# Performance work log

Measured on AMD Instinct MI355X. Metric: run time of the kernel, lower is better.

Reference implementation:

```python
import jax, jax.numpy as jnp
import numpy as np

WIN = (16, 9, 9)
WIN_SIZE = WIN[0] * WIN[1] * WIN[2]  # 1296
EPS = float(np.e ** -15)             # ~3.06e-7, matches np.power(np.e, -15)


def setup_inputs() -> dict:
    key = jax.random.key(0)
    k1, k2 = jax.random.split(key)
    shape = (2, 1, 96, 192, 192)  # [B, 1, D, H, W]
    I = jax.random.normal(k1, shape, dtype=jnp.float32)
    J = jax.random.normal(k2, shape, dtype=jnp.float32)
    return {"I": I, "J": J}


def _box_sums(tmp):
    # Grouped conv3d with an all-ones [5,1,16,9,9] kernel: per-channel sliding
    k = jnp.ones((5, 1) + WIN, dtype=tmp.dtype)
    return jax.lax.conv_general_dilated(
        tmp, k,
        window_strides=(1, 1, 1),
        padding=[(0, 0), (WIN[1] // 2, WIN[1] // 2), (WIN[2] // 2, WIN[2] // 2)],
        feature_group_count=5,
        dimension_numbers=("NCDHW", "OIDHW", "NCDHW"),
    )


def reference(I, J):
    # I, J: [B, 1, D, H, W]
    tmp = jnp.concatenate([I, J, I * I, J * J, I * J], axis=1)  # [B,5,D,H,W]
    sums = _box_sums(tmp)  # [B, 5, D-15, H, W]
    I_sum, J_sum = sums[:, 0], sums[:, 1]
    I2_sum, J2_sum, IJ_sum = sums[:, 2], sums[:, 3], sums[:, 4]

    u_I = I_sum / WIN_SIZE
    u_J = J_sum / WIN_SIZE

    cross = IJ_sum - u_J * I_sum - u_I * J_sum + u_I * u_J * WIN_SIZE
    I_var = I2_sum - 2.0 * u_I * I_sum + u_I * u_I * WIN_SIZE
    J_var = J2_sum - 2.0 * u_J * J_sum + u_J * u_J * WIN_SIZE

    nz = (I_var * J_var) > EPS  # bool_non_zero; where false, substitute 1.0
    cross = jnp.where(nz, cross, 1.0)
    I_var = jnp.where(nz, I_var, 1.0)
    J_var = jnp.where(nz, J_var, 1.0)

    cc = cross * cross / (I_var * J_var + EPS)  # [B, D-15, H, W]
    loss = -1.0 * jnp.mean(cc, axis=(1, 2, 3)) + 1.0  # [B]
    return loss, cc
```

## Files before the change

### kernel.cpp

```cpp
#include <hip/hip_runtime.h>


constexpr int N = 2, D = 96, H = 192, W = 192;
constexpr int OD = 81;
constexpr int KD = 16;
constexpr int HWp = H * W;
constexpr float INV_WIN = 1.0f / 1296.0f;
constexpr float EPS_NZ = 3.0590232050182579e-07f;
constexpr int CH = 24;
constexpr int ODPB = 27;

__device__ __forceinline__ unsigned bf16rne(float f) {
  unsigned u = __float_as_uint(f);
  return (u + 0x7fffu + ((u >> 16) & 1u)) >> 16;
}
__device__ __forceinline__ float bf16tof(unsigned h) {
  return __uint_as_float(h << 16);
}

__global__ __launch_bounds__(192)
void k_dw(const float* __restrict__ I, const float* __restrict__ J,
          unsigned* __restrict__ ws, int od0, int c, int odcStride) {
  const int h = blockIdx.x;
  const int n = blockIdx.z;
  const int os = od0 + blockIdx.y * ODPB;
  int oe = od0 + c; if (os + ODPB < oe) oe = os + ODPB;
  if (os >= oe) return;
  const int w = threadIdx.x;

  __shared__ float4 x4[W + 8];
  __shared__ float  x1[W + 8];
  __shared__ float4 a4[W + 8];
  __shared__ float  a1[W + 8];

  if (w < 4)       { x4[w]     = make_float4(0.f,0.f,0.f,0.f); x1[w]     = 0.f; }
  if (w >= W - 4)  { x4[w + 8] = make_float4(0.f,0.f,0.f,0.f); x1[w + 8] = 0.f; }
  __syncthreads();

  const size_t colBase = ((size_t)n * D * H + h) * (size_t)W + w;
  const float* Ip = I + colBase;
  const float* Jp = J + colBase;
  unsigned* wbase = ws + ((size_t)n * odcStride * HWp + (size_t)h * W + w) * 3;

  int pe = -1;
  if (w < 3) pe = w + 1;
  else if (w >= W - 3) pe = w + 7;

  const int dEnd = oe + KD - 1;
  float sI = 0.f, sJ = 0.f, sII = 0.f, sJJ = 0.f, sIJ = 0.f;
  float ivN = Ip[(size_t)os * HWp];
  float jvN = Jp[(size_t)os * HWp];
  float ioN = 0.f, joN = 0.f;

  for (int d = os; d < dEnd; ++d) {
    const float iv = ivN, jv = jvN;
    const float io = ioN, jo = joN;
    const int dn = d + 1;
    if (dn < dEnd) {
      ivN = Ip[(size_t)dn * HWp];
      jvN = Jp[(size_t)dn * HWp];
      if (dn >= os + KD - 1) {
        const int odn = dn - (KD - 1);
        ioN = Ip[(size_t)odn * HWp];
        joN = Jp[(size_t)odn * HWp];
      }
    }
    sI += iv; sJ += jv;
    sII += iv * iv; sJJ += jv * jv; sIJ += iv * jv;
    if (d >= os + KD - 1) {
      const int od = d - (KD - 1);
      const int p = 4 + w;
      __builtin_amdgcn_s_barrier();
      x4[p] = make_float4(sI, sJ, sII, sJJ); x1[p] = sIJ;
      asm volatile("s_waitcnt lgkmcnt(0)" ::: "memory");
      __builtin_amdgcn_s_barrier();
      {
        float4 m0 = x4[p - 1], m1 = x4[p], m2 = x4[p + 1];
        a4[p] = make_float4(m0.x + m1.x + m2.x, m0.y + m1.y + m2.y,
                            m0.z + m1.z + m2.z, m0.w + m1.w + m2.w);
        a1[p] = x1[p - 1] + x1[p] + x1[p + 1];
        if (pe >= 0) {
          float4 e0 = x4[pe - 1], e1 = x4[pe], e2 = x4[pe + 1];
          a4[pe] = make_float4(e0.x + e1.x + e2.x, e0.y + e1.y + e2.y,
                               e0.z + e1.z + e2.z, e0.w + e1.w + e2.w);
          a1[pe] = x1[pe - 1] + x1[pe] + x1[pe + 1];
        }
      }
      asm volatile("s_waitcnt lgkmcnt(0)" ::: "memory");
      __builtin_amdgcn_s_barrier();
      float4 b0 = a4[p - 3], b1 = a4[p], b2 = a4[p + 3];
      const float r0 = b0.x + b1.x + b2.x;
      const float r1 = b0.y + b1.y + b2.y;
      const float r2 = b0.z + b1.z + b2.z;
      const float r3 = b0.w + b1.w + b2.w;
      const float r4 = a1[p - 3] + a1[p] + a1[p + 3];
      unsigned* o = wbase + (size_t)(od - od0) * HWp * 3;
      uint3 v = make_uint3(bf16rne(r0) | (bf16rne(r1) << 16),
                           bf16rne(r2) | (bf16rne(r3) << 16),
                           bf16rne(r4));
      *(uint3*)o = v;
      sI -= io; sJ -= jo;
      sII -= io * io; sJJ -= jo * jo; sIJ -= io * jo;
    }
  }
}

__global__ __launch_bounds__(192)
void k_hcc(const unsigned* __restrict__ ws, float* __restrict__ cc,
           float* __restrict__ acc, int od0, int odcStride) {
  const int odi = blockIdx.x;
  const int od = od0 + odi;
  const int h0 = blockIdx.y * CH;
  const int n = blockIdx.z;
  const int w = threadIdx.x;
  const unsigned* base =
      ws + ((size_t)n * odcStride * HWp + (size_t)odi * HWp + w) * 3;
  float* ccp = cc + ((size_t)n * OD + od) * (size_t)HWp + w;

  float s0 = 0.f, s1 = 0.f, s2 = 0.f, s3 = 0.f, s4 = 0.f;
  float lsum = 0.f;
  uint3 hist[8];
  const uint3 z3 = make_uint3(0u, 0u, 0u);

  uint3 vN = z3;
  {
    const int hin = h0 - 4;
    if (hin >= 0) vN = *(const uint3*)(base + (size_t)hin * W * 3);
  }
#pragma unroll
  for (int t = 0; t < CH + 8; ++t) {
    const uint3 v = vN;
    if (t + 1 < CH + 8) {
      const int hn = h0 - 4 + t + 1;
      vN = (hn >= 0 && hn < H) ? *(const uint3*)(base + (size_t)hn * W * 3) : z3;
    }
    s0 += bf16tof(v.x & 0xffffu); s1 += bf16tof(v.x >> 16);
    s2 += bf16tof(v.y & 0xffffu); s3 += bf16tof(v.y >> 16);
    s4 += bf16tof(v.z & 0xffffu);
    if (t >= 8) {
      const int h = h0 + t - 8;
      const float cross = s4 - s0 * s1 * INV_WIN;
      const float vI = s2 - s0 * s0 * INV_WIN;
      const float vJ = s3 - s1 * s1 * INV_WIN;
      const float prod = vI * vJ;
      const float c = (prod > EPS_NZ) ? (cross * cross) / (prod + EPS_NZ)
                                      : 1.0f / (1.0f + EPS_NZ);
      ccp[(size_t)h * W] = c;
      lsum += c;
      const uint3 q = hist[t & 7];
      s0 -= bf16tof(q.x & 0xffffu); s1 -= bf16tof(q.x >> 16);
      s2 -= bf16tof(q.y & 0xffffu); s3 -= bf16tof(q.y >> 16);
      s4 -= bf16tof(q.z & 0xffffu);
    }
    hist[t & 7] = v;
  }
  __shared__ float red[3];
#pragma unroll
  for (int off = 32; off > 0; off >>= 1) lsum += __shfl_xor(lsum, off, 64);
  if ((threadIdx.x & 63) == 0) red[threadIdx.x >> 6] = lsum;
  __syncthreads();
  if (threadIdx.x == 0) atomicAdd(acc + n, red[0] + red[1] + red[2]);
}

__global__ void k_fin(const float* __restrict__ acc, float* __restrict__ out) {
  if (threadIdx.x < N)
    out[threadIdx.x] = 1.0f - acc[threadIdx.x] * (1.0f / 2985984.0f);
}

extern "C" void kernel_launch(void* const* d_in, const int* in_sizes, int n_in,
                              void* d_out, int out_size, void* d_ws,
                              size_t ws_size, hipStream_t stream) {
  const float* I = (const float*)d_in[0];
  const float* J = (const float*)d_in[1];
  float* out = (float*)d_out;
  float* acc = (float*)d_ws;
  unsigned* planes = (unsigned*)((char*)d_ws + 256);

  hipMemsetAsync(d_ws, 0, 2 * sizeof(float), stream);

  const size_t perOdPerN = (size_t)HWp * 12;
  size_t avail = (ws_size > 256) ? (ws_size - 256) : 0;
  long long odcMax = (long long)(avail / (2 * perOdPerN));
  if (odcMax < 1) odcMax = 1;
  if (odcMax > OD) odcMax = OD;
  const int odc = (int)odcMax;

  float* ccOut = out + 2;
  for (int od0 = 0; od0 < OD; od0 += odc) {
    const int c = (odc < OD - od0) ? odc : (OD - od0);
    const int S = (c + ODPB - 1) / ODPB;
    hipLaunchKernelGGL(k_dw, dim3(H, S, N), dim3(192), 0, stream,
                       I, J, planes, od0, c, odc);
    hipLaunchKernelGGL(k_hcc, dim3(c, H / CH, N), dim3(192), 0, stream,
                       planes, ccOut, acc, od0, odc);
  }
  hipLaunchKernelGGL(k_fin, dim3(1), dim3(64), 0, stream, acc, out);
}
```

Measured before the change: 78.79 us.

## Use fp16 packed sums and wave bpermute for W-direction box filter

```diff
diff --git a/kernel.cpp b/kernel.cpp
--- a/kernel.cpp
+++ b/kernel.cpp
@@ -8,17 +8,25 @@
 constexpr float INV_WIN = 1.0f / 1296.0f;
 constexpr float EPS_NZ = 3.0590232050182579e-07f;
 constexpr int CH = 24;
-constexpr int ODPB = 27;
+constexpr int ODPB = 14;
 
-__device__ __forceinline__ unsigned bf16rne(float f) {
-  unsigned u = __float_as_uint(f);
-  return (u + 0x7fffu + ((u >> 16) & 1u)) >> 16;
+typedef __fp16 h2 __attribute__((ext_vector_type(2)));
+
+__device__ __forceinline__ unsigned pkrtz(float lo, float hi) {
+  h2 h = __builtin_amdgcn_cvt_pkrtz(lo, hi);
+  unsigned u; __builtin_memcpy(&u, &h, 4); return u;
 }
-__device__ __forceinline__ float bf16tof(unsigned h) {
-  return __uint_as_float(h << 16);
+__device__ __forceinline__ h2 as_h2(unsigned u) {
+  h2 h; __builtin_memcpy(&h, &u, 4); return h;
+}
+__device__ __forceinline__ unsigned as_u(h2 h) {
+  unsigned u; __builtin_memcpy(&u, &h, 4); return u;
+}
+__device__ __forceinline__ unsigned bperm(int bidx, unsigned v) {
+  return (unsigned)__builtin_amdgcn_ds_bpermute(bidx, (int)v);
 }
 
-__global__ __launch_bounds__(192)
+__global__ __launch_bounds__(256)
 void k_dw(const float* __restrict__ I, const float* __restrict__ J,
           unsigned* __restrict__ ws, int od0, int c, int odcStride) {
   const int h = blockIdx.x;
@@ -26,81 +34,63 @@
   const int os = od0 + blockIdx.y * ODPB;
   int oe = od0 + c; if (os + ODPB < oe) oe = os + ODPB;
   if (os >= oe) return;
-  const int w = threadIdx.x;
 
-  __shared__ float4 x4[W + 8];
-  __shared__ float  x1[W + 8];
-  __shared__ float4 a4[W + 8];
-  __shared__ float  a1[W + 8];
+  const int lane = threadIdx.x & 63;
+  const int seg  = threadIdx.x >> 6;
+  const int wcol = seg * 56 + lane - 4;
+  const bool colOK = (wcol >= 0) && (wcol < W);
+  const bool stOK  = (lane >= 4) && (lane < 60) && (wcol < W);
 
-  if (w < 4)       { x4[w]     = make_float4(0.f,0.f,0.f,0.f); x1[w]     = 0.f; }
-  if (w >= W - 4)  { x4[w + 8] = make_float4(0.f,0.f,0.f,0.f); x1[w + 8] = 0.f; }
-  __syncthreads();
-
-  const size_t colBase = ((size_t)n * D * H + h) * (size_t)W + w;
+  const size_t colBase = ((size_t)n * D * H + h) * (size_t)W + wcol;
   const float* Ip = I + colBase;
   const float* Jp = J + colBase;
-  unsigned* wbase = ws + ((size_t)n * odcStride * HWp + (size_t)h * W + w) * 3;
+  unsigned* wbase = ws + ((size_t)n * odcStride * HWp + (size_t)h * W + wcol) * 3;
 
-  int pe = -1;
-  if (w < 3) pe = w + 1;
-  else if (w >= W - 3) pe = w + 7;
+  const int im1 = ((lane - 1) & 63) << 2;
+  const int ip1 = ((lane + 1) & 63) << 2;
+  const int im3 = ((lane - 3) & 63) << 2;
+  const int ip3 = ((lane + 3) & 63) << 2;
 
-  const int dEnd = oe + KD - 1;
   float sI = 0.f, sJ = 0.f, sII = 0.f, sJJ = 0.f, sIJ = 0.f;
-  float ivN = Ip[(size_t)os * HWp];
-  float jvN = Jp[(size_t)os * HWp];
-  float ioN = 0.f, joN = 0.f;
-
-  for (int d = os; d < dEnd; ++d) {
-    const float iv = ivN, jv = jvN;
-    const float io = ioN, jo = joN;
-    const int dn = d + 1;
-    if (dn < dEnd) {
-      ivN = Ip[(size_t)dn * HWp];
-      jvN = Jp[(size_t)dn * HWp];
-      if (dn >= os + KD - 1) {
-        const int odn = dn - (KD - 1);
-        ioN = Ip[(size_t)odn * HWp];
-        joN = Jp[(size_t)odn * HWp];
-      }
-    }
+  for (int d = os; d < os + KD - 1; ++d) {
+    const float iv = colOK ? Ip[(size_t)d * HWp] : 0.f;
+    const float jv = colOK ? Jp[(size_t)d * HWp] : 0.f;
     sI += iv; sJ += jv;
     sII += iv * iv; sJJ += jv * jv; sIJ += iv * jv;
-    if (d >= os + KD - 1) {
-      const int od = d - (KD - 1);
-      const int p = 4 + w;
-      __builtin_amdgcn_s_barrier();
-      x4[p] = make_float4(sI, sJ, sII, sJJ); x1[p] = sIJ;
-      asm volatile("s_waitcnt lgkmcnt(0)" ::: "memory");
-      __builtin_amdgcn_s_barrier();
-      {
-        float4 m0 = x4[p - 1], m1 = x4[p], m2 = x4[p + 1];
-        a4[p] = make_float4(m0.x + m1.x + m2.x, m0.y + m1.y + m2.y,
-                            m0.z + m1.z + m2.z, m0.w + m1.w + m2.w);
-        a1[p] = x1[p - 1] + x1[p] + x1[p + 1];
-        if (pe >= 0) {
-          float4 e0 = x4[pe - 1], e1 = x4[pe], e2 = x4[pe + 1];
-          a4[pe] = make_float4(e0.x + e1.x + e2.x, e0.y + e1.y + e2.y,
-                               e0.z + e1.z + e2.z, e0.w + e1.w + e2.w);
-          a1[pe] = x1[pe - 1] + x1[pe] + x1[pe + 1];
-        }
-      }
-      asm volatile("s_waitcnt lgkmcnt(0)" ::: "memory");
-      __builtin_amdgcn_s_barrier();
-      float4 b0 = a4[p - 3], b1 = a4[p], b2 = a4[p + 3];
-      const float r0 = b0.x + b1.x + b2.x;
-      const float r1 = b0.y + b1.y + b2.y;
-      const float r2 = b0.z + b1.z + b2.z;
-      const float r3 = b0.w + b1.w + b2.w;
-      const float r4 = a1[p - 3] + a1[p] + a1[p + 3];
+  }
+
+  float eI = colOK ? Ip[(size_t)(os + KD - 1) * HWp] : 0.f;
+  float eJ = colOK ? Jp[(size_t)(os + KD - 1) * HWp] : 0.f;
+  float lI = colOK ? Ip[(size_t)os * HWp] : 0.f;
+  float lJ = colOK ? Jp[(size_t)os * HWp] : 0.f;
+
+  for (int od = os; od < oe; ++od) {
+    const float ceI = eI, ceJ = eJ, clI = lI, clJ = lJ;
+    const int odn = od + 1;
+    if (odn < oe) {
+      eI = colOK ? Ip[(size_t)(odn + KD - 1) * HWp] : 0.f;
+      eJ = colOK ? Jp[(size_t)(odn + KD - 1) * HWp] : 0.f;
+      lI = colOK ? Ip[(size_t)odn * HWp] : 0.f;
+      lJ = colOK ? Jp[(size_t)odn * HWp] : 0.f;
+    }
+    sI += ceI; sJ += ceJ;
+    sII += ceI * ceI; sJJ += ceJ * ceJ; sIJ += ceI * ceJ;
+    const unsigned x0 = pkrtz(sI, sJ);
+    const unsigned x1 = pkrtz(sII, sJJ);
+    const unsigned x2 = pkrtz(sIJ, 0.f);
+    sI -= clI; sJ -= clJ;
+    sII -= clI * clI; sJJ -= clJ * clJ; sIJ -= clI * clJ;
+
+    const unsigned a0 = as_u(as_h2(bperm(im1, x0)) + as_h2(x0) + as_h2(bperm(ip1, x0)));
+    const unsigned a1 = as_u(as_h2(bperm(im1, x1)) + as_h2(x1) + as_h2(bperm(ip1, x1)));
+    const unsigned a2 = as_u(as_h2(bperm(im1, x2)) + as_h2(x2) + as_h2(bperm(ip1, x2)));
+    const unsigned r0 = as_u(as_h2(bperm(im3, a0)) + as_h2(a0) + as_h2(bperm(ip3, a0)));
+    const unsigned r1 = as_u(as_h2(bperm(im3, a1)) + as_h2(a1) + as_h2(bperm(ip3, a1)));
+    const unsigned r2 = as_u(as_h2(bperm(im3, a2)) + as_h2(a2) + as_h2(bperm(ip3, a2)));
+
+    if (stOK) {
       unsigned* o = wbase + (size_t)(od - od0) * HWp * 3;
-      uint3 v = make_uint3(bf16rne(r0) | (bf16rne(r1) << 16),
-                           bf16rne(r2) | (bf16rne(r3) << 16),
-                           bf16rne(r4));
-      *(uint3*)o = v;
-      sI -= io; sJ -= jo;
-      sII -= io * io; sJJ -= jo * jo; sIJ -= io * jo;
+      o[0] = r0; o[1] = r1; o[2] = r2;
     }
   }
 }
@@ -134,9 +124,12 @@
       const int hn = h0 - 4 + t + 1;
       vN = (hn >= 0 && hn < H) ? *(const uint3*)(base + (size_t)hn * W * 3) : z3;
     }
-    s0 += bf16tof(v.x & 0xffffu); s1 += bf16tof(v.x >> 16);
-    s2 += bf16tof(v.y & 0xffffu); s3 += bf16tof(v.y >> 16);
-    s4 += bf16tof(v.z & 0xffffu);
+    {
+      h2 v0 = as_h2(v.x), v1 = as_h2(v.y), v2 = as_h2(v.z);
+      s0 += (float)v0[0]; s1 += (float)v0[1];
+      s2 += (float)v1[0]; s3 += (float)v1[1];
+      s4 += (float)v2[0];
+    }
     if (t >= 8) {
       const int h = h0 + t - 8;
       const float cross = s4 - s0 * s1 * INV_WIN;
@@ -148,9 +141,10 @@
       ccp[(size_t)h * W] = c;
       lsum += c;
       const uint3 q = hist[t & 7];
-      s0 -= bf16tof(q.x & 0xffffu); s1 -= bf16tof(q.x >> 16);
-      s2 -= bf16tof(q.y & 0xffffu); s3 -= bf16tof(q.y >> 16);
-      s4 -= bf16tof(q.z & 0xffffu);
+      h2 q0 = as_h2(q.x), q1 = as_h2(q.y), q2 = as_h2(q.z);
+      s0 -= (float)q0[0]; s1 -= (float)q0[1];
+      s2 -= (float)q1[0]; s3 -= (float)q1[1];
+      s4 -= (float)q2[0];
     }
     hist[t & 7] = v;
   }
@@ -189,7 +183,7 @@
   for (int od0 = 0; od0 < OD; od0 += odc) {
     const int c = (odc < OD - od0) ? odc : (OD - od0);
     const int S = (c + ODPB - 1) / ODPB;
-    hipLaunchKernelGGL(k_dw, dim3(H, S, N), dim3(192), 0, stream,
+    hipLaunchKernelGGL(k_dw, dim3(H, S, N), dim3(256), 0, stream,
                        I, J, planes, od0, c, odc);
     hipLaunchKernelGGL(k_hcc, dim3(c, H / CH, N), dim3(192), 0, stream,
                        planes, ccOut, acc, od0, odc);
```

Result: faster. 76.73 us (-2.6%).

## Move W-direction box sum from depth kernel into H/cc kernel, split atomics

Applied to the files above, without the earlier changes.

```diff
diff --git a/kernel.cpp b/kernel.cpp
--- a/kernel.cpp
+++ b/kernel.cpp
@@ -8,7 +8,7 @@
 constexpr float INV_WIN = 1.0f / 1296.0f;
 constexpr float EPS_NZ = 3.0590232050182579e-07f;
 constexpr int CH = 24;
-constexpr int ODPB = 27;
+constexpr int ODPB = 14;
 
 __device__ __forceinline__ unsigned bf16rne(float f) {
   unsigned u = __float_as_uint(f);
@@ -19,8 +19,8 @@
 }
 
 __global__ __launch_bounds__(192)
-void k_dw(const float* __restrict__ I, const float* __restrict__ J,
-          unsigned* __restrict__ ws, int od0, int c, int odcStride) {
+void k_d(const float* __restrict__ I, const float* __restrict__ J,
+         unsigned* __restrict__ ws, int od0, int c, int odcStride) {
   const int h = blockIdx.x;
   const int n = blockIdx.z;
   const int os = od0 + blockIdx.y * ODPB;
@@ -28,86 +28,56 @@
   if (os >= oe) return;
   const int w = threadIdx.x;
 
-  __shared__ float4 x4[W + 8];
-  __shared__ float  x1[W + 8];
-  __shared__ float4 a4[W + 8];
-  __shared__ float  a1[W + 8];
-
-  if (w < 4)       { x4[w]     = make_float4(0.f,0.f,0.f,0.f); x1[w]     = 0.f; }
-  if (w >= W - 4)  { x4[w + 8] = make_float4(0.f,0.f,0.f,0.f); x1[w + 8] = 0.f; }
-  __syncthreads();
-
   const size_t colBase = ((size_t)n * D * H + h) * (size_t)W + w;
   const float* Ip = I + colBase;
   const float* Jp = J + colBase;
   unsigned* wbase = ws + ((size_t)n * odcStride * HWp + (size_t)h * W + w) * 3;
 
-  int pe = -1;
-  if (w < 3) pe = w + 1;
-  else if (w >= W - 3) pe = w + 7;
-
-  const int dEnd = oe + KD - 1;
   float sI = 0.f, sJ = 0.f, sII = 0.f, sJJ = 0.f, sIJ = 0.f;
-  float ivN = Ip[(size_t)os * HWp];
-  float jvN = Jp[(size_t)os * HWp];
-  float ioN = 0.f, joN = 0.f;
-
-  for (int d = os; d < dEnd; ++d) {
-    const float iv = ivN, jv = jvN;
-    const float io = ioN, jo = joN;
-    const int dn = d + 1;
-    if (dn < dEnd) {
-      ivN = Ip[(size_t)dn * HWp];
-      jvN = Jp[(size_t)dn * HWp];
-      if (dn >= os + KD - 1) {
-        const int odn = dn - (KD - 1);
-        ioN = Ip[(size_t)odn * HWp];
-        joN = Jp[(size_t)odn * HWp];
-      }
-    }
+  for (int d = os; d < os + KD - 1; ++d) {
+    const float iv = Ip[(size_t)d * HWp];
+    const float jv = Jp[(size_t)d * HWp];
     sI += iv; sJ += jv;
     sII += iv * iv; sJJ += jv * jv; sIJ += iv * jv;
-    if (d >= os + KD - 1) {
-      const int od = d - (KD - 1);
-      const int p = 4 + w;
-      __builtin_amdgcn_s_barrier();
-      x4[p] = make_float4(sI, sJ, sII, sJJ); x1[p] = sIJ;
-      asm volatile("s_waitcnt lgkmcnt(0)" ::: "memory");
-      __builtin_amdgcn_s_barrier();
-      {
-        float4 m0 = x4[p - 1], m1 = x4[p], m2 = x4[p + 1];
-        a4[p] = make_float4(m0.x + m1.x + m2.x, m0.y + m1.y + m2.y,
-                            m0.z + m1.z + m2.z, m0.w + m1.w + m2.w);
-        a1[p] = x1[p - 1] + x1[p] + x1[p + 1];
-        if (pe >= 0) {
-          float4 e0 = x4[pe - 1], e1 = x4[pe], e2 = x4[pe + 1];
-          a4[pe] = make_float4(e0.x + e1.x + e2.x, e0.y + e1.y + e2.y,
-                               e0.z + e1.z + e2.z, e0.w + e1.w + e2.w);
-          a1[pe] = x1[pe - 1] + x1[pe] + x1[pe + 1];
-        }
-      }
-      asm volatile("s_waitcnt lgkmcnt(0)" ::: "memory");
-      __builtin_amdgcn_s_barrier();
-      float4 b0 = a4[p - 3], b1 = a4[p], b2 = a4[p + 3];
-      const float r0 = b0.x + b1.x + b2.x;
-      const float r1 = b0.y + b1.y + b2.y;
-      const float r2 = b0.z + b1.z + b2.z;
-      const float r3 = b0.w + b1.w + b2.w;
-      const float r4 = a1[p - 3] + a1[p] + a1[p + 3];
-      unsigned* o = wbase + (size_t)(od - od0) * HWp * 3;
-      uint3 v = make_uint3(bf16rne(r0) | (bf16rne(r1) << 16),
-                           bf16rne(r2) | (bf16rne(r3) << 16),
-                           bf16rne(r4));
-      *(uint3*)o = v;
-      sI -= io; sJ -= jo;
-      sII -= io * io; sJJ -= jo * jo; sIJ -= io * jo;
-    }
-  }
+  }
+
+#define ISSUE1(e_, f_, g_, h_, O)                                            \
+  { const int _o = (O);                                                      \
+    if (_o < oe) {                                                           \
+      e_ = Ip[(size_t)(_o + KD - 1) * HWp];                                  \
+      f_ = Jp[(size_t)(_o + KD - 1) * HWp];                                  \
+      g_ = Ip[(size_t)_o * HWp];                                             \
+      h_ = Jp[(size_t)_o * HWp]; } }
+
+#define STEP1(O, e_, f_, g_, h_)                                             \
+  { const int _od = (O);                                                     \
+    sI += e_; sJ += f_;                                                      \
+    sII += e_ * e_; sJJ += f_ * f_; sIJ += e_ * f_;                          \
+    unsigned* o = wbase + (size_t)(_od - od0) * HWp * 3;                     \
+    *(uint3*)o = make_uint3(bf16rne(sI) | (bf16rne(sJ) << 16),               \
+                            bf16rne(sII) | (bf16rne(sJJ) << 16),             \
+                            bf16rne(sIJ));                                   \
+    sI -= g_; sJ -= h_;                                                      \
+    sII -= g_ * g_; sJJ -= h_ * h_; sIJ -= g_ * h_; }
+
+  float eA=0,fA=0,gA=0,hA=0, eB=0,fB=0,gB=0,hB=0;
+  ISSUE1(eA, fA, gA, hA, os)
+  ISSUE1(eB, fB, gB, hB, os + 1)
+  for (int od = os; od < oe; od += 2) {
+    STEP1(od, eA, fA, gA, hA)
+    ISSUE1(eA, fA, gA, hA, od + 2)
+    if (od + 1 < oe) {
+      STEP1(od + 1, eB, fB, gB, hB)
+      ISSUE1(eB, fB, gB, hB, od + 3)
+    }
+  }
+#undef ISSUE1
+#undef STEP1
 }
 
 __global__ __launch_bounds__(192)
-void k_hcc(const unsigned* __restrict__ ws, float* __restrict__ cc,
-           float* __restrict__ acc, int od0, int odcStride) {
+void k_whcc(const unsigned* __restrict__ ws, float* __restrict__ cc,
+            float* __restrict__ acc, int od0, int odcStride) {
   const int odi = blockIdx.x;
   const int od = od0 + odi;
   const int h0 = blockIdx.y * CH;
@@ -117,6 +87,19 @@
       ws + ((size_t)n * odcStride * HWp + (size_t)odi * HWp + w) * 3;
   float* ccp = cc + ((size_t)n * OD + od) * (size_t)HWp + w;
 
+  __shared__ unsigned xw0[W + 8], xw1[W + 8], xw2[W + 8];
+  __shared__ float4 a4[W + 8];
+  __shared__ float  a1[W + 8];
+
+  if (w < 4) { xw0[w] = 0u; xw1[w] = 0u; xw2[w] = 0u; }
+  if (w >= W - 4) { xw0[w + 8] = 0u; xw1[w + 8] = 0u; xw2[w + 8] = 0u; }
+  __syncthreads();
+
+  int pe = -1;
+  if (w < 3) pe = w + 1;
+  else if (w >= W - 3) pe = w + 7;
+  const int p = 4 + w;
+
   float s0 = 0.f, s1 = 0.f, s2 = 0.f, s3 = 0.f, s4 = 0.f;
   float lsum = 0.f;
   uint3 hist[8];
@@ -134,37 +117,76 @@
       const int hn = h0 - 4 + t + 1;
       vN = (hn >= 0 && hn < H) ? *(const uint3*)(base + (size_t)hn * W * 3) : z3;
     }
-    s0 += bf16tof(v.x & 0xffffu); s1 += bf16tof(v.x >> 16);
-    s2 += bf16tof(v.y & 0xffffu); s3 += bf16tof(v.y >> 16);
-    s4 += bf16tof(v.z & 0xffffu);
+    xw0[p] = v.x; xw1[p] = v.y; xw2[p] = v.z;
+    asm volatile("s_waitcnt lgkmcnt(0)" ::: "memory");
+    __builtin_amdgcn_s_barrier();
+    const unsigned m0 = xw0[p - 1], m1 = xw1[p - 1], m2 = xw2[p - 1];
+    const unsigned q0 = xw0[p + 1], q1 = xw1[p + 1], q2 = xw2[p + 1];
+    const float A0 = bf16tof(m0 & 0xffffu) + bf16tof(v.x & 0xffffu) + bf16tof(q0 & 0xffffu);
+    const float A1 = bf16tof(m0 >> 16)     + bf16tof(v.x >> 16)     + bf16tof(q0 >> 16);
+    const float A2 = bf16tof(m1 & 0xffffu) + bf16tof(v.y & 0xffffu) + bf16tof(q1 & 0xffffu);
+    const float A3 = bf16tof(m1 >> 16)     + bf16tof(v.y >> 16)     + bf16tof(q1 >> 16);
+    const float A4 = bf16tof(m2 & 0xffffu) + bf16tof(v.z & 0xffffu) + bf16tof(q2 & 0xffffu);
+    a4[p] = make_float4(A0, A1, A2, A3); a1[p] = A4;
+    if (pe >= 0) {
+      const unsigned e0 = xw0[pe - 1], e1 = xw1[pe - 1], e2 = xw2[pe - 1];
+      const unsigned c0 = xw0[pe],     c1 = xw1[pe],     c2 = xw2[pe];
+      const unsigned g0 = xw0[pe + 1], g1 = xw1[pe + 1], g2 = xw2[pe + 1];
+      a4[pe] = make_float4(
+        bf16tof(e0 & 0xffffu) + bf16tof(c0 & 0xffffu) + bf16tof(g0 & 0xffffu),
+        bf16tof(e0 >> 16)     + bf16tof(c0 >> 16)     + bf16tof(g0 >> 16),
+        bf16tof(e1 & 0xffffu) + bf16tof(c1 & 0xffffu) + bf16tof(g1 & 0xffffu),
+        bf16tof(e1 >> 16)     + bf16tof(c1 >> 16)     + bf16tof(g1 >> 16));
+      a1[pe] = bf16tof(e2 & 0xffffu) + bf16tof(c2 & 0xffffu) + bf16tof(g2 & 0xffffu);
+    }
+    asm volatile("s_waitcnt lgkmcnt(0)" ::: "memory");
+    __builtin_amdgcn_s_barrier();
+    const float4 bm = a4[p - 3]; const float em = a1[p - 3];
+    const float4 bp = a4[p + 3]; const float ep = a1[p + 3];
+    const float r0 = bm.x + A0 + bp.x;
+    const float r1 = bm.y + A1 + bp.y;
+    const float r2 = bm.z + A2 + bp.z;
+    const float r3 = bm.w + A3 + bp.w;
+    const float r4 = em + A4 + ep;
+    const uint3 pk = make_uint3(bf16rne(r0) | (bf16rne(r1) << 16),
+                                bf16rne(r2) | (bf16rne(r3) << 16),
+                                bf16rne(r4));
+    s0 += bf16tof(pk.x & 0xffffu); s1 += bf16tof(pk.x >> 16);
+    s2 += bf16tof(pk.y & 0xffffu); s3 += bf16tof(pk.y >> 16);
+    s4 += bf16tof(pk.z & 0xffffu);
     if (t >= 8) {
       const int h = h0 + t - 8;
       const float cross = s4 - s0 * s1 * INV_WIN;
       const float vI = s2 - s0 * s0 * INV_WIN;
       const float vJ = s3 - s1 * s1 * INV_WIN;
       const float prod = vI * vJ;
-      const float c = (prod > EPS_NZ) ? (cross * cross) / (prod + EPS_NZ)
-                                      : 1.0f / (1.0f + EPS_NZ);
-      ccp[(size_t)h * W] = c;
-      lsum += c;
+      const float cv = (prod > EPS_NZ) ? (cross * cross) / (prod + EPS_NZ)
+                                       : 1.0f / (1.0f + EPS_NZ);
+      ccp[(size_t)h * W] = cv;
+      lsum += cv;
       const uint3 q = hist[t & 7];
       s0 -= bf16tof(q.x & 0xffffu); s1 -= bf16tof(q.x >> 16);
       s2 -= bf16tof(q.y & 0xffffu); s3 -= bf16tof(q.y >> 16);
       s4 -= bf16tof(q.z & 0xffffu);
     }
-    hist[t & 7] = v;
+    hist[t & 7] = pk;
   }
   __shared__ float red[3];
 #pragma unroll
   for (int off = 32; off > 0; off >>= 1) lsum += __shfl_xor(lsum, off, 64);
   if ((threadIdx.x & 63) == 0) red[threadIdx.x >> 6] = lsum;
   __syncthreads();
-  if (threadIdx.x == 0) atomicAdd(acc + n, red[0] + red[1] + red[2]);
+  if (threadIdx.x == 0)
+    atomicAdd(acc + n * 32 + (odi & 31), red[0] + red[1] + red[2]);
 }
 
 __global__ void k_fin(const float* __restrict__ acc, float* __restrict__ out) {
-  if (threadIdx.x < N)
-    out[threadIdx.x] = 1.0f - acc[threadIdx.x] * (1.0f / 2985984.0f);
+  const int t = threadIdx.x;
+  float v = acc[t];
+#pragma unroll
+  for (int off = 16; off > 0; off >>= 1) v += __shfl_xor(v, off, 32);
+  if (t == 0)  out[0] = 1.0f - v * (1.0f / 2985984.0f);
+  if (t == 32) out[1] = 1.0f - v * (1.0f / 2985984.0f);
 }
 
 extern "C" void kernel_launch(void* const* d_in, const int* in_sizes, int n_in,
@@ -176,7 +198,7 @@
   float* acc = (float*)d_ws;
   unsigned* planes = (unsigned*)((char*)d_ws + 256);
 
-  hipMemsetAsync(d_ws, 0, 2 * sizeof(float), stream);
+  hipMemsetAsync(d_ws, 0, 64 * sizeof(float), stream);
 
   const size_t perOdPerN = (size_t)HWp * 12;
   size_t avail = (ws_size > 256) ? (ws_size - 256) : 0;
@@ -189,9 +211,9 @@
   for (int od0 = 0; od0 < OD; od0 += odc) {
     const int c = (odc < OD - od0) ? odc : (OD - od0);
     const int S = (c + ODPB - 1) / ODPB;
-    hipLaunchKernelGGL(k_dw, dim3(H, S, N), dim3(192), 0, stream,
+    hipLaunchKernelGGL(k_d, dim3(H, S, N), dim3(192), 0, stream,
                        I, J, planes, od0, c, odc);
-    hipLaunchKernelGGL(k_hcc, dim3(c, H / CH, N), dim3(192), 0, stream,
+    hipLaunchKernelGGL(k_whcc, dim3(c, H / CH, N), dim3(192), 0, stream,
                        planes, ccOut, acc, od0, odc);
   }
   hipLaunchKernelGGL(k_fin, dim3(1), dim3(64), 0, stream, acc, out);
```

After: 85.72 us. 8.8% more time.
